# Kernel optimization log

Measured on AMD Instinct MI355X. Metric: run time of the kernel, lower is better.

## Reference

```python
import jax, jax.numpy as jnp
import numpy as np

N, P, T, D = 25000, 100000, 4, 128
DIN = 4 * D + 4  # 516
LEAKY = 0.001


def setup_inputs() -> dict:
    key = jax.random.key(0)
    ks = jax.random.split(key, 12)
    inp = {
        "coords": jax.random.normal(ks[0], (N, T, 3), jnp.float32),
        "propers": jax.random.randint(ks[1], (P, 4), 0, N, jnp.int64),
        "encoded": jax.random.normal(ks[2], (N, D), jnp.float32),
        "t": jax.random.uniform(ks[3], (T,), jnp.float32),
        "answer": jax.random.normal(ks[4], (N, T, 3), jnp.float32),
        # AggregateMLP(516 -> 128 -> 128 -> 128 -> 2), LeakyReLU(0.001) between
        "W0": jax.random.normal(ks[5], (DIN, D), jnp.float32) / np.sqrt(DIN),
        "b0": jnp.zeros((D,), jnp.float32),
        "W1": jax.random.normal(ks[6], (D, D), jnp.float32) / np.sqrt(D),
        "b1": jnp.zeros((D,), jnp.float32),
        "W2": jax.random.normal(ks[7], (D, D), jnp.float32) / np.sqrt(D),
        "b2": jnp.zeros((D,), jnp.float32),
        "W3": jax.random.normal(ks[8], (D, 2), jnp.float32) / np.sqrt(D),
        "b3": jnp.zeros((2,), jnp.float32),
    }
    return inp


def _forward(coords, propers, encoded, t, answer, W0, b0, W1, b1, W2, b2, W3, b3):
    p0, p1, p2, p3 = propers[:, 0], propers[:, 1], propers[:, 2], propers[:, 3]
    c0, c1, c2, c3 = coords[p0], coords[p1], coords[p2], coords[p3]  # [P,T,3]
    u1 = c1 - c0
    u2 = c2 - c1
    u3 = c3 - c2
    u1xu2 = jnp.cross(u1, u2, axis=-1)
    u2xu3 = jnp.cross(u2, u3, axis=-1)
    u2_norm = jnp.linalg.norm(u2, axis=-1, keepdims=True)
    u1yu2 = u1 * u2_norm
    theta = jnp.arctan2((u1yu2 * u2xu3).sum(-1), (u1xu2 * u2xu3).sum(-1))  # [P,T]
    dr = c0 - c3  # [P,T,3]
    dl = jnp.sqrt(jnp.clip(jnp.square(dr).sum(-1), 1e-12))  # [P,T]
    dh = dr / dl[..., None]

    Pn, Tn = propers.shape[0], t.shape[0]
    bcast = lambda e: jnp.broadcast_to(e[:, None, :], (Pn, Tn, e.shape[-1]))
    feats = jnp.concatenate(
        [
            bcast(encoded[p0]),
            bcast(encoded[p1]),
            bcast(encoded[p2]),
            bcast(encoded[p3]),
            jnp.broadcast_to(t.reshape(1, Tn, 1), (Pn, Tn, 1)),
            jnp.sin(theta)[..., None],
            jnp.cos(theta)[..., None],
            dl[..., None],
        ],
        axis=2,
    )  # [P,T,516]

    h = jax.nn.leaky_relu(feats @ W0 + b0, LEAKY)
    h = jax.nn.leaky_relu(h @ W1 + b1, LEAKY)
    h = jax.nn.leaky_relu(h @ W2 + b2, LEAKY)
    delta = h @ W3 + b3  # [P,T,2]

    out = answer.at[p0].add(-0.5 * delta[:, :, 0:1] * dh)
    out = out.at[p3].add(0.5 * delta[:, :, 1:2] * dh)
    return out


def reference(coords, propers, encoded, t, answer, W0, b0, W1, b1, W2, b2, W3, b3):
    return _forward(coords, propers, encoded, t, answer, W0, b0, W1, b1, W2, b2, W3, b3)
```

## Files before the change

kernel.cpp:

```cpp
#include <hip/hip_runtime.h>
#include <hip/hip_bf16.h>

#define NN 25000
#define PP 100000
#define TT 4
#define DD 128
#define LEAKY 0.001f

#define PB 32
#define ROWS 128

typedef __bf16 bf16;
typedef __bf16 bf16x8 __attribute__((ext_vector_type(8)));
typedef float  f32x4  __attribute__((ext_vector_type(4)));
typedef float  f32x2  __attribute__((ext_vector_type(2)));

#define OFF_W0SW  0u
#define OFF_W1SW  131072u
#define OFF_W2SW  163840u
#define OFF_W3SW  196608u
#define OFF_WTB   200704u
#define OFF_W5B   201728u
#define OFF_E     202496u
#define WS_END    25802496u

#define PR_W0SW  8192
#define PR_W1SW  2048
#define PR_W2SW  2048
#define PR_W3SW  256
#define PR_WTB   64
#define PR_W5B   48
#define PR_COPY4 75000
#define PR_TOTAL (PR_W0SW + PR_W1SW + PR_W2SW + PR_W3SW + PR_WTB + PR_W5B + PR_COPY4)

#define LGKM0() asm volatile("s_waitcnt lgkmcnt(0)" ::: "memory")

__device__ __forceinline__ void gload_lds16(const void* g, void* l) {
    __builtin_amdgcn_global_load_lds(
        (const __attribute__((address_space(1))) void*)g,
        (__attribute__((address_space(3))) void*)l, 16, 0, 0);
}

__global__ __launch_bounds__(256) void prep_kernel(
    const float* __restrict__ W0, const float* __restrict__ W1,
    const float* __restrict__ W2, const float* __restrict__ W3,
    const float* __restrict__ answer, const float* __restrict__ tvec,
    const float* __restrict__ b0,
    bf16* __restrict__ W0sw, bf16* __restrict__ W1sw, bf16* __restrict__ W2sw,
    bf16* __restrict__ W3sw, bf16* __restrict__ WtB, bf16* __restrict__ W5B,
    float* __restrict__ out)
{
    int idx = blockIdx.x * 256 + threadIdx.x;
    if (idx < PR_W0SW) {
        int lane = idx & 63, c = idx >> 6;
        int fr = lane & 15, quad = lane >> 4;
        int kc = c & 15, iwv = c >> 4;
        bf16 v[8];
        #pragma unroll
        for (int j = 0; j < 8; ++j)
            v[j] = (bf16)W0[(kc * 32 + quad * 8 + j) * 128 + iwv * 16 + fr];
        *(bf16x8*)(W0sw + c * 512 + lane * 8) = *(const bf16x8*)v;
        return;
    }
    idx -= PR_W0SW;
    if (idx < PR_W1SW) {
        int lane = idx & 63, c = idx >> 6;
        int fr = lane & 15, quad = lane >> 4;
        int kc = c & 3, nt = c >> 2;
        bf16 v[8];
        #pragma unroll
        for (int j = 0; j < 8; ++j)
            v[j] = (bf16)W1[(kc * 32 + quad * 8 + j) * 128 + nt * 16 + fr];
        *(bf16x8*)(W1sw + c * 512 + lane * 8) = *(const bf16x8*)v;
        return;
    }
    idx -= PR_W1SW;
    if (idx < PR_W2SW) {
        int lane = idx & 63, c = idx >> 6;
        int fr = lane & 15, quad = lane >> 4;
        int kc = c & 3, nt = c >> 2;
        bf16 v[8];
        #pragma unroll
        for (int j = 0; j < 8; ++j)
            v[j] = (bf16)W2[(kc * 32 + quad * 8 + j) * 128 + nt * 16 + fr];
        *(bf16x8*)(W2sw + c * 512 + lane * 8) = *(const bf16x8*)v;
        return;
    }
    idx -= PR_W2SW;
    if (idx < PR_W3SW) {
        int lane = idx & 63, kc = idx >> 6;
        int fr = lane & 15, quad = lane >> 4;
        bf16 v[8];
        #pragma unroll
        for (int j = 0; j < 8; ++j)
            v[j] = (fr < 2) ? (bf16)W3[(kc * 32 + quad * 8 + j) * 2 + fr] : (bf16)0.0f;
        *(bf16x8*)(W3sw + kc * 512 + lane * 8) = *(const bf16x8*)v;
        return;
    }
    idx -= PR_W3SW;
    if (idx < PR_WTB) {
        int t = idx >> 4, s = idx & 15;
        float tv = tvec[t];
        bf16 v[8];
        #pragma unroll
        for (int j = 0; j < 8; ++j)
            v[j] = (bf16)(tv * W0[512 * 128 + s * 8 + j] + b0[s * 8 + j]);
        *(bf16x8*)(WtB + t * 128 + s * 8) = *(const bf16x8*)v;
        return;
    }
    idx -= PR_WTB;
    if (idx < PR_W5B) {
        int r = idx >> 4, s = idx & 15;
        bf16 v[8];
        #pragma unroll
        for (int j = 0; j < 8; ++j)
            v[j] = (bf16)W0[(513 + r) * 128 + s * 8 + j];
        *(bf16x8*)(W5B + r * 128 + s * 8) = *(const bf16x8*)v;
        return;
    }
    idx -= PR_W5B;
    if (idx < PR_COPY4) { ((float4*)out)[idx] = ((const float4*)answer)[idx]; }
}

__global__ __launch_bounds__(256) void prep_e_kernel(
    const float* __restrict__ encoded, const bf16* __restrict__ W0sw,
    bf16* __restrict__ E)
{
    __shared__ bf16 sA[64][136];
    __shared__ bf16 sT[64][40];
    const int tid = threadIdx.x;
    const int row0 = (blockIdx.x >> 2) * 64;
    const int ntb  = blockIdx.x & 3;
    for (int c = tid; c < 2048; c += 256) {
        int row = c >> 5, seg = c & 31;
        int rr = row0 + row; if (rr >= NN) rr = NN - 1;
        float4 v = *(const float4*)(encoded + (size_t)rr * 128 + seg * 4);
        bf16 pk[4] = {(bf16)v.x, (bf16)v.y, (bf16)v.z, (bf16)v.w};
        *(uint2*)(&sA[row][seg * 4]) = *(const uint2*)pk;
    }
    __syncthreads();
    const int wv = tid >> 6, lane = tid & 63;
    const int fr = lane & 15, quad = lane >> 4;
    const bf16* aBase = &sA[wv * 16 + fr][quad * 8];
    bf16x8 aFv[4];
    #pragma unroll
    for (int kcc = 0; kcc < 4; ++kcc) aFv[kcc] = *(const bf16x8*)(aBase + kcc * 32);
    const int orow = tid >> 2, oseg = tid & 3;
    #pragma unroll
    for (int i = 0; i < 4; ++i) {
        #pragma unroll
        for (int ntl = 0; ntl < 2; ++ntl) {
            int nt = ntb * 2 + ntl;
            f32x4 acc = {0.f, 0.f, 0.f, 0.f};
            #pragma unroll
            for (int kcc = 0; kcc < 4; ++kcc) {
                bf16x8 bF = *(const bf16x8*)(W0sw + ((size_t)nt * 16 + i * 4 + kcc) * 512 + lane * 8);
                acc = __builtin_amdgcn_mfma_f32_16x16x32_bf16(aFv[kcc], bF, acc, 0, 0, 0);
            }
            #pragma unroll
            for (int reg = 0; reg < 4; ++reg)
                sT[wv * 16 + quad * 4 + reg][ntl * 16 + fr] = (bf16)acc[reg];
        }
        LGKM0();
        bf16x8 ev = *(const bf16x8*)(&sT[orow][oseg * 8]);
        LGKM0();
        if (row0 + orow < NN)
            *(bf16x8*)(E + ((size_t)i * NN + row0 + orow) * 128 + ntb * 32 + oseg * 8) = ev;
    }
}

__global__ __launch_bounds__(512, 4) void main_kernel(
    const float* __restrict__ coords, const int* __restrict__ propers,
    const float* __restrict__ b1, const float* __restrict__ b2,
    const float* __restrict__ b3,
    const bf16* __restrict__ E, const bf16* __restrict__ W1sw,
    const bf16* __restrict__ W2sw, const bf16* __restrict__ W3sw,
    const bf16* __restrict__ WtB, const bf16* __restrict__ W5B,
    float* __restrict__ out)
{
    __shared__ __align__(16) bf16 sH[8][16][136];
    __shared__ __align__(16) bf16 sW[18432];
    __shared__ float sScr[8][16][6];
    __shared__ int   sNd[8][8];

    const int tid  = threadIdx.x;
    const int wv   = tid >> 6, lane = tid & 63;
    const int fr   = lane & 15, quad = lane >> 4;
    const int pw   = blockIdx.x * PB + wv * 4;

    {
        const char* g1 = (const char*)W1sw;
        char* l = (char*)&sW[0];
        #pragma unroll
        for (int r2 = 0; r2 < 4; ++r2)
            gload_lds16(g1 + r2 * 8192 + wv * 1024 + lane * 16,
                        l + r2 * 8192 + wv * 1024);
        if (wv < 4)
            gload_lds16((const char*)W3sw + wv * 1024 + lane * 16,
                        l + 32768 + wv * 1024);
    }

    int4 pv = *(const int4*)(propers + (size_t)(pw + quad) * 4);
    bf16x8 e0 = *(const bf16x8*)(E + ((size_t)0 * NN + pv.x) * 128 + fr * 8);
    bf16x8 e1 = *(const bf16x8*)(E + ((size_t)1 * NN + pv.y) * 128 + fr * 8);
    bf16x8 e2 = *(const bf16x8*)(E + ((size_t)2 * NN + pv.z) * 128 + fr * 8);
    bf16x8 e3 = *(const bf16x8*)(E + ((size_t)3 * NN + pv.w) * 128 + fr * 8);
    if (fr == 0) { sNd[wv][quad * 2] = pv.x; sNd[wv][quad * 2 + 1] = pv.w; }
    bf16x8 w3v = *(const bf16x8*)(W5B + 0 * 128 + fr * 8);
    bf16x8 w4v = *(const bf16x8*)(W5B + 1 * 128 + fr * 8);
    bf16x8 w5v = *(const bf16x8*)(W5B + 2 * 128 + fr * 8);

    float b1r[8], b2r[8];
    #pragma unroll
    for (int i = 0; i < 8; ++i) {
        b1r[i] = b1[i * 16 + fr];
        b2r[i] = b2[i * 16 + fr];
    }
    float b3r = (fr < 2) ? b3[fr] : 0.0f;

    float snl = 0.f, csl = 1.f, dll = 0.f;
    if (lane < 16) {
        int pp_ = lane >> 2, t = lane & 3;
        int4 pg = *(const int4*)(propers + (size_t)(pw + pp_) * 4);
        const float* c0 = coords + (size_t)pg.x * 12 + t * 3;
        const float* c1 = coords + (size_t)pg.y * 12 + t * 3;
        const float* c2 = coords + (size_t)pg.z * 12 + t * 3;
        const float* c3 = coords + (size_t)pg.w * 12 + t * 3;
        float u1x = c1[0]-c0[0], u1y = c1[1]-c0[1], u1z = c1[2]-c0[2];
        float u2x = c2[0]-c1[0], u2y = c2[1]-c1[1], u2z = c2[2]-c1[2];
        float u3x = c3[0]-c2[0], u3y = c3[1]-c2[1], u3z = c3[2]-c2[2];
        float ax = u1y*u2z - u1z*u2y, ay = u1z*u2x - u1x*u2z, az = u1x*u2y - u1y*u2x;
        float bx = u2y*u3z - u2z*u3y, by = u2z*u3x - u2x*u3z, bz = u2x*u3y - u2y*u3x;
        float u2n = sqrtf(u2x*u2x + u2y*u2y + u2z*u2z);
        float num = u2n * (u1x*bx + u1y*by + u1z*bz);
        float den = ax*bx + ay*by + az*bz;
        float hyp = sqrtf(num*num + den*den);
        if (hyp > 1e-30f) { float ih = 1.0f / hyp; snl = num * ih; csl = den * ih; }
        else { snl = 0.0f; csl = 1.0f; }
        float drx = c0[0]-c3[0], dry = c0[1]-c3[1], drz = c0[2]-c3[2];
        dll = sqrtf(fmaxf(drx*drx + dry*dry + drz*drz, 1e-12f));
        float il = 1.0f / dll;
        sScr[wv][lane][0] = drx * il;
        sScr[wv][lane][1] = dry * il;
        sScr[wv][lane][2] = drz * il;
    }

    {
        f32x2 g2[4], w3f2[4], w4f2[4], w5f2[4];
        #pragma unroll
        for (int j = 0; j < 4; ++j) {
            g2[j] = (f32x2){
                (float)e0[2*j]   + (float)e1[2*j]   + (float)e2[2*j]   + (float)e3[2*j],
                (float)e0[2*j+1] + (float)e1[2*j+1] + (float)e2[2*j+1] + (float)e3[2*j+1] };
            w3f2[j] = (f32x2){ (float)w3v[2*j], (float)w3v[2*j+1] };
            w4f2[j] = (f32x2){ (float)w4v[2*j], (float)w4v[2*j+1] };
            w5f2[j] = (f32x2){ (float)w5v[2*j], (float)w5v[2*j+1] };
        }
        #pragma unroll
        for (int t = 0; t < 4; ++t) {
            int r = quad * 4 + t;
            bf16x8 wtv = *(const bf16x8*)(WtB + t * 128 + fr * 8);
            float sn = __shfl(snl, r), cs = __shfl(csl, r), dl = __shfl(dll, r);
            f32x2 sn2 = {sn, sn}, cs2 = {cs, cs}, dl2 = {dl, dl};
            bf16 hv[8];
            #pragma unroll
            for (int j = 0; j < 4; ++j) {
                f32x2 v = g2[j] + (f32x2){ (float)wtv[2*j], (float)wtv[2*j+1] };
                v = sn2 * w3f2[j] + v;
                v = cs2 * w4f2[j] + v;
                v = dl2 * w5f2[j] + v;
                f32x2 lv = v * LEAKY;
                v.x = fmaxf(v.x, lv.x);
                v.y = fmaxf(v.y, lv.y);
                hv[2*j]   = (bf16)v.x;
                hv[2*j+1] = (bf16)v.y;
            }
            *(bf16x8*)(&sH[wv][r][fr * 8]) = *(const bf16x8*)hv;
        }
    }
    __syncthreads();

#define DENSE_LAYER(BR)                                                         \
    {                                                                           \
        bf16x8 aF[4];                                                           \
        const bf16* aRow = &sH[wv][fr][quad * 8];                               \
        _Pragma("unroll")                                                       \
        for (int kc = 0; kc < 4; ++kc)                                          \
            aF[kc] = *(const bf16x8*)(aRow + kc * 32);                          \
        _Pragma("unroll")                                                       \
        for (int hh = 0; hh < 2; ++hh) {                                        \
            f32x4 acc[4];                                                       \
            _Pragma("unroll")                                                   \
            for (int nt = 0; nt < 4; ++nt) acc[nt] = (f32x4){0.f,0.f,0.f,0.f};  \
            __builtin_amdgcn_s_setprio(1);                                      \
            _Pragma("unroll")                                                   \
            for (int kc = 0; kc < 4; ++kc) {                                    \
                _Pragma("unroll")                                               \
                for (int nt = 0; nt < 4; ++nt) {                                \
                    bf16x8 bF = *(const bf16x8*)(sW +                           \
                        ((hh * 4 + nt) * 4 + kc) * 512 + lane * 8);             \
                    acc[nt] = __builtin_amdgcn_mfma_f32_16x16x32_bf16(          \
                        aF[kc], bF, acc[nt], 0, 0, 0);                          \
                }                                                               \
            }                                                                   \
            __builtin_amdgcn_s_setprio(0);                                      \
            _Pragma("unroll")                                                   \
            for (int nt = 0; nt < 4; ++nt) {                                    \
                int j = (hh * 4 + nt) * 16 + fr;                                \
                f32x4 v = acc[nt] + BR[hh * 4 + nt];                            \
                f32x4 lv = v * LEAKY;                                           \
                v.x = fmaxf(v.x, lv.x); v.y = fmaxf(v.y, lv.y);                 \
                v.z = fmaxf(v.z, lv.z); v.w = fmaxf(v.w, lv.w);                 \
                _Pragma("unroll")                                               \
                for (int reg = 0; reg < 4; ++reg)                               \
                    sH[wv][quad * 4 + reg][j] = (bf16)v[reg];                   \
            }                                                                   \
        }                                                                       \
    }

    DENSE_LAYER(b1r)
    __syncthreads();
    {
        const char* g2 = (const char*)W2sw;
        char* l = (char*)&sW[0];
        #pragma unroll
        for (int r2 = 0; r2 < 4; ++r2)
            gload_lds16(g2 + r2 * 8192 + wv * 1024 + lane * 16,
                        l + r2 * 8192 + wv * 1024);
    }
    __syncthreads();
    DENSE_LAYER(b2r)

    {
        bf16x8 aF[4];
        const bf16* aRow = &sH[wv][fr][quad * 8];
        #pragma unroll
        for (int kc = 0; kc < 4; ++kc)
            aF[kc] = *(const bf16x8*)(aRow + kc * 32);
        f32x4 dacc = {0.f, 0.f, 0.f, 0.f};
        __builtin_amdgcn_s_setprio(1);
        #pragma unroll
        for (int kc = 0; kc < 4; ++kc) {
            bf16x8 bF = *(const bf16x8*)(sW + 16384 + kc * 512 + lane * 8);
            dacc = __builtin_amdgcn_mfma_f32_16x16x32_bf16(aF[kc], bF, dacc, 0, 0, 0);
        }
        __builtin_amdgcn_s_setprio(0);
        if (fr < 2) {
            #pragma unroll
            for (int reg = 0; reg < 4; ++reg)
                sScr[wv][quad * 4 + reg][3 + fr] = dacc[reg] + b3r;
        }
    }

    {
        int row = lane & 15;
        int comp = lane >> 4;
        int side = (comp == 3) ? 1 : 0;
        int ax = side ? 0 : comp;
        int node = sNd[wv][(row >> 2) * 2 + side];
        float dval = (side ? 0.5f : -0.5f) * sScr[wv][row][3 + side];
        atomicAdd(out + (size_t)node * 12 + (row & 3) * 3 + ax, dval * sScr[wv][row][ax]);
        if (lane < 32) {
            int ax2 = 1 + comp;
            int node2 = sNd[wv][(row >> 2) * 2 + 1];
            float dval2 = 0.5f * sScr[wv][row][4];
            atomicAdd(out + (size_t)node2 * 12 + (row & 3) * 3 + ax2, dval2 * sScr[wv][row][ax2]);
        }
    }
#undef DENSE_LAYER
}

extern "C" void kernel_launch(void* const* d_in, const int* in_sizes, int n_in,
                              void* d_out, int out_size, void* d_ws, size_t ws_size,
                              hipStream_t stream) {
    const float* coords  = (const float*)d_in[0];
    const int*   propers = (const int*)d_in[1];
    const float* encoded = (const float*)d_in[2];
    const float* tvec    = (const float*)d_in[3];
    const float* answer  = (const float*)d_in[4];
    const float* W0 = (const float*)d_in[5];
    const float* b0 = (const float*)d_in[6];
    const float* W1 = (const float*)d_in[7];
    const float* b1 = (const float*)d_in[8];
    const float* W2 = (const float*)d_in[9];
    const float* b2 = (const float*)d_in[10];
    const float* W3 = (const float*)d_in[11];
    const float* b3 = (const float*)d_in[12];
    float* out = (float*)d_out;
    char* ws = (char*)d_ws;
    bf16* W0sw = (bf16*)(ws + OFF_W0SW);
    bf16* W1sw = (bf16*)(ws + OFF_W1SW);
    bf16* W2sw = (bf16*)(ws + OFF_W2SW);
    bf16* W3sw = (bf16*)(ws + OFF_W3SW);
    bf16* WtB  = (bf16*)(ws + OFF_WTB);
    bf16* W5B  = (bf16*)(ws + OFF_W5B);
    bf16* E    = (bf16*)(ws + OFF_E);

    int prep_blocks = (PR_TOTAL + 255) / 256;
    prep_kernel<<<prep_blocks, 256, 0, stream>>>(W0, W1, W2, W3, answer, tvec, b0,
                                                 W0sw, W1sw, W2sw, W3sw, WtB, W5B, out);
    prep_e_kernel<<<391 * 4, 256, 0, stream>>>(encoded, W0sw, E);
    main_kernel<<<PP / PB, 512, 0, stream>>>(coords, propers, b1, b2, b3,
                                             E, W1sw, W2sw, W3sw, WtB, W5B, out);
}
```

Measured before the change: 166.5 us.

## Make main kernel persistent with resident weights and prefetched next-chunk gathers

The main kernel now runs as a fixed grid of 256 blocks that loop over chunks of propers. All of W1, W2 and W3 are loaded into a larger LDS buffer once per block, which removes the per-block weight reloads and the mid-kernel barriers around the W2 swap. The propers indices, embedding rows and coordinates for the next chunk are issued before the current chunk's dense layers, so gather latency overlaps with MFMA work. In exchange there are fewer resident waves per CU, more register pressure, and a fixed grid size that may not balance evenly across CUs.

```diff
diff --git a/kernel.cpp b/kernel.cpp
--- a/kernel.cpp
+++ b/kernel.cpp
@@ -169,7 +169,7 @@
     }
 }
 
-__global__ __launch_bounds__(512, 4) void main_kernel(
+__global__ __launch_bounds__(512, 2) void main_kernel(
     const float* __restrict__ coords, const int* __restrict__ propers,
     const float* __restrict__ b1, const float* __restrict__ b2,
     const float* __restrict__ b3,
@@ -179,36 +179,17 @@
     float* __restrict__ out)
 {
     __shared__ __align__(16) bf16 sH[8][16][136];
-    __shared__ __align__(16) bf16 sW[18432];
+    __shared__ __align__(16) bf16 sW[34816];
     __shared__ float sScr[8][16][6];
     __shared__ int   sNd[8][8];
 
     const int tid  = threadIdx.x;
     const int wv   = tid >> 6, lane = tid & 63;
     const int fr   = lane & 15, quad = lane >> 4;
-    const int pw   = blockIdx.x * PB + wv * 4;
-
-    {
-        const char* g1 = (const char*)W1sw;
-        char* l = (char*)&sW[0];
-        #pragma unroll
-        for (int r2 = 0; r2 < 4; ++r2)
-            gload_lds16(g1 + r2 * 8192 + wv * 1024 + lane * 16,
-                        l + r2 * 8192 + wv * 1024);
-        if (wv < 4)
-            gload_lds16((const char*)W3sw + wv * 1024 + lane * 16,
-                        l + 32768 + wv * 1024);
-    }
-
-    int4 pv = *(const int4*)(propers + (size_t)(pw + quad) * 4);
-    bf16x8 e0 = *(const bf16x8*)(E + ((size_t)0 * NN + pv.x) * 128 + fr * 8);
-    bf16x8 e1 = *(const bf16x8*)(E + ((size_t)1 * NN + pv.y) * 128 + fr * 8);
-    bf16x8 e2 = *(const bf16x8*)(E + ((size_t)2 * NN + pv.z) * 128 + fr * 8);
-    bf16x8 e3 = *(const bf16x8*)(E + ((size_t)3 * NN + pv.w) * 128 + fr * 8);
-    if (fr == 0) { sNd[wv][quad * 2] = pv.x; sNd[wv][quad * 2 + 1] = pv.w; }
-    bf16x8 w3v = *(const bf16x8*)(W5B + 0 * 128 + fr * 8);
-    bf16x8 w4v = *(const bf16x8*)(W5B + 1 * 128 + fr * 8);
-    bf16x8 w5v = *(const bf16x8*)(W5B + 2 * 128 + fr * 8);
+
+    for (int i = wv; i < 68; i += 8)
+        gload_lds16((const char*)W1sw + (size_t)i * 1024 + lane * 16,
+                    (char*)sW + i * 1024);
 
     float b1r[8], b2r[8];
     #pragma unroll
@@ -217,70 +198,132 @@
         b2r[i] = b2[i * 16 + fr];
     }
     float b3r = (fr < 2) ? b3[fr] : 0.0f;
-
-    float snl = 0.f, csl = 1.f, dll = 0.f;
-    if (lane < 16) {
-        int pp_ = lane >> 2, t = lane & 3;
-        int4 pg = *(const int4*)(propers + (size_t)(pw + pp_) * 4);
-        const float* c0 = coords + (size_t)pg.x * 12 + t * 3;
-        const float* c1 = coords + (size_t)pg.y * 12 + t * 3;
-        const float* c2 = coords + (size_t)pg.z * 12 + t * 3;
-        const float* c3 = coords + (size_t)pg.w * 12 + t * 3;
-        float u1x = c1[0]-c0[0], u1y = c1[1]-c0[1], u1z = c1[2]-c0[2];
-        float u2x = c2[0]-c1[0], u2y = c2[1]-c1[1], u2z = c2[2]-c1[2];
-        float u3x = c3[0]-c2[0], u3y = c3[1]-c2[1], u3z = c3[2]-c2[2];
-        float ax = u1y*u2z - u1z*u2y, ay = u1z*u2x - u1x*u2z, az = u1x*u2y - u1y*u2x;
-        float bx = u2y*u3z - u2z*u3y, by = u2z*u3x - u2x*u3z, bz = u2x*u3y - u2y*u3x;
-        float u2n = sqrtf(u2x*u2x + u2y*u2y + u2z*u2z);
-        float num = u2n * (u1x*bx + u1y*by + u1z*bz);
-        float den = ax*bx + ay*by + az*bz;
-        float hyp = sqrtf(num*num + den*den);
-        if (hyp > 1e-30f) { float ih = 1.0f / hyp; snl = num * ih; csl = den * ih; }
-        else { snl = 0.0f; csl = 1.0f; }
-        float drx = c0[0]-c3[0], dry = c0[1]-c3[1], drz = c0[2]-c3[2];
-        dll = sqrtf(fmaxf(drx*drx + dry*dry + drz*drz, 1e-12f));
-        float il = 1.0f / dll;
-        sScr[wv][lane][0] = drx * il;
-        sScr[wv][lane][1] = dry * il;
-        sScr[wv][lane][2] = drz * il;
-    }
-
+    bf16x8 w3v = *(const bf16x8*)(W5B + 0 * 128 + fr * 8);
+    bf16x8 w4v = *(const bf16x8*)(W5B + 1 * 128 + fr * 8);
+    bf16x8 w5v = *(const bf16x8*)(W5B + 2 * 128 + fr * 8);
+    bf16x8 wtv[4];
+    #pragma unroll
+    for (int t = 0; t < 4; ++t) wtv[t] = *(const bf16x8*)(WtB + t * 128 + fr * 8);
+    f32x2 w3f2[4], w4f2[4], w5f2[4];
+    #pragma unroll
+    for (int j = 0; j < 4; ++j) {
+        w3f2[j] = (f32x2){ (float)w3v[2*j], (float)w3v[2*j+1] };
+        w4f2[j] = (f32x2){ (float)w4v[2*j], (float)w4v[2*j+1] };
+        w5f2[j] = (f32x2){ (float)w5v[2*j], (float)w5v[2*j+1] };
+    }
+
+    __syncthreads();
+
+    const int nChunks = PP / PB;
+    const int stride  = gridDim.x;
+    int chunk = blockIdx.x;
+
+    int4 pv; bf16x8 e0, e1, e2, e3; float cc[12];
     {
-        f32x2 g2[4], w3f2[4], w4f2[4], w5f2[4];
-        #pragma unroll
-        for (int j = 0; j < 4; ++j) {
-            g2[j] = (f32x2){
-                (float)e0[2*j]   + (float)e1[2*j]   + (float)e2[2*j]   + (float)e3[2*j],
-                (float)e0[2*j+1] + (float)e1[2*j+1] + (float)e2[2*j+1] + (float)e3[2*j+1] };
-            w3f2[j] = (f32x2){ (float)w3v[2*j], (float)w3v[2*j+1] };
-            w4f2[j] = (f32x2){ (float)w4v[2*j], (float)w4v[2*j+1] };
-            w5f2[j] = (f32x2){ (float)w5v[2*j], (float)w5v[2*j+1] };
-        }
-        #pragma unroll
-        for (int t = 0; t < 4; ++t) {
-            int r = quad * 4 + t;
-            bf16x8 wtv = *(const bf16x8*)(WtB + t * 128 + fr * 8);
-            float sn = __shfl(snl, r), cs = __shfl(csl, r), dl = __shfl(dll, r);
-            f32x2 sn2 = {sn, sn}, cs2 = {cs, cs}, dl2 = {dl, dl};
-            bf16 hv[8];
-            #pragma unroll
-            for (int j = 0; j < 4; ++j) {
-                f32x2 v = g2[j] + (f32x2){ (float)wtv[2*j], (float)wtv[2*j+1] };
-                v = sn2 * w3f2[j] + v;
-                v = cs2 * w4f2[j] + v;
-                v = dl2 * w5f2[j] + v;
-                f32x2 lv = v * LEAKY;
-                v.x = fmaxf(v.x, lv.x);
-                v.y = fmaxf(v.y, lv.y);
-                hv[2*j]   = (bf16)v.x;
-                hv[2*j+1] = (bf16)v.y;
-            }
-            *(bf16x8*)(&sH[wv][r][fr * 8]) = *(const bf16x8*)hv;
-        }
-    }
-    __syncthreads();
-
-#define DENSE_LAYER(BR)                                                         \
+        int pw = chunk * PB + wv * 4;
+        pv = *(const int4*)(propers + (size_t)(pw + quad) * 4);
+        e0 = *(const bf16x8*)(E + ((size_t)0 * NN + pv.x) * 128 + fr * 8);
+        e1 = *(const bf16x8*)(E + ((size_t)1 * NN + pv.y) * 128 + fr * 8);
+        e2 = *(const bf16x8*)(E + ((size_t)2 * NN + pv.z) * 128 + fr * 8);
+        e3 = *(const bf16x8*)(E + ((size_t)3 * NN + pv.w) * 128 + fr * 8);
+        if (lane < 16) {
+            int4 pg = *(const int4*)(propers + (size_t)(pw + (lane >> 2)) * 4);
+            int t = lane & 3;
+            const float* q0 = coords + (size_t)pg.x * 12 + t * 3;
+            const float* q1 = coords + (size_t)pg.y * 12 + t * 3;
+            const float* q2 = coords + (size_t)pg.z * 12 + t * 3;
+            const float* q3 = coords + (size_t)pg.w * 12 + t * 3;
+            cc[0]=q0[0]; cc[1]=q0[1]; cc[2]=q0[2];
+            cc[3]=q1[0]; cc[4]=q1[1]; cc[5]=q1[2];
+            cc[6]=q2[0]; cc[7]=q2[1]; cc[8]=q2[2];
+            cc[9]=q3[0]; cc[10]=q3[1]; cc[11]=q3[2];
+        }
+    }
+
+    while (true) {
+        const int next = chunk + stride;
+        const bool more = next < nChunks;
+
+        int4 pvn, pgn;
+        if (more) {
+            int pwn = next * PB + wv * 4;
+            pvn = *(const int4*)(propers + (size_t)(pwn + quad) * 4);
+            if (lane < 16)
+                pgn = *(const int4*)(propers + (size_t)(pwn + (lane >> 2)) * 4);
+        }
+
+        if (fr == 0) { sNd[wv][quad * 2] = pv.x; sNd[wv][quad * 2 + 1] = pv.w; }
+
+        float snl = 0.f, csl = 1.f, dll = 0.f;
+        if (lane < 16) {
+            float u1x = cc[3]-cc[0], u1y = cc[4]-cc[1], u1z = cc[5]-cc[2];
+            float u2x = cc[6]-cc[3], u2y = cc[7]-cc[4], u2z = cc[8]-cc[5];
+            float u3x = cc[9]-cc[6], u3y = cc[10]-cc[7], u3z = cc[11]-cc[8];
+            float ax = u1y*u2z - u1z*u2y, ay = u1z*u2x - u1x*u2z, az = u1x*u2y - u1y*u2x;
+            float bx = u2y*u3z - u2z*u3y, by = u2z*u3x - u2x*u3z, bz = u2x*u3y - u2y*u3x;
+            float u2n = sqrtf(u2x*u2x + u2y*u2y + u2z*u2z);
+            float num = u2n * (u1x*bx + u1y*by + u1z*bz);
+            float den = ax*bx + ay*by + az*bz;
+            float hyp = sqrtf(num*num + den*den);
+            if (hyp > 1e-30f) { float ih = 1.0f / hyp; snl = num * ih; csl = den * ih; }
+            else { snl = 0.0f; csl = 1.0f; }
+            float drx = cc[0]-cc[9], dry = cc[1]-cc[10], drz = cc[2]-cc[11];
+            dll = sqrtf(fmaxf(drx*drx + dry*dry + drz*drz, 1e-12f));
+            float il = 1.0f / dll;
+            sScr[wv][lane][0] = drx * il;
+            sScr[wv][lane][1] = dry * il;
+            sScr[wv][lane][2] = drz * il;
+        }
+
+        {
+            f32x2 g2[4];
+            #pragma unroll
+            for (int j = 0; j < 4; ++j)
+                g2[j] = (f32x2){
+                    (float)e0[2*j]   + (float)e1[2*j]   + (float)e2[2*j]   + (float)e3[2*j],
+                    (float)e0[2*j+1] + (float)e1[2*j+1] + (float)e2[2*j+1] + (float)e3[2*j+1] };
+            #pragma unroll
+            for (int t = 0; t < 4; ++t) {
+                int r = quad * 4 + t;
+                float sn = __shfl(snl, r), cs = __shfl(csl, r), dl = __shfl(dll, r);
+                f32x2 sn2 = {sn, sn}, cs2 = {cs, cs}, dl2 = {dl, dl};
+                bf16 hv[8];
+                #pragma unroll
+                for (int j = 0; j < 4; ++j) {
+                    f32x2 v = g2[j] + (f32x2){ (float)wtv[t][2*j], (float)wtv[t][2*j+1] };
+                    v = sn2 * w3f2[j] + v;
+                    v = cs2 * w4f2[j] + v;
+                    v = dl2 * w5f2[j] + v;
+                    f32x2 lv = v * LEAKY;
+                    v.x = fmaxf(v.x, lv.x);
+                    v.y = fmaxf(v.y, lv.y);
+                    hv[2*j]   = (bf16)v.x;
+                    hv[2*j+1] = (bf16)v.y;
+                }
+                *(bf16x8*)(&sH[wv][r][fr * 8]) = *(const bf16x8*)hv;
+            }
+        }
+
+        bf16x8 e0n, e1n, e2n, e3n; float ccn[12];
+        if (more) {
+            e0n = *(const bf16x8*)(E + ((size_t)0 * NN + pvn.x) * 128 + fr * 8);
+            e1n = *(const bf16x8*)(E + ((size_t)1 * NN + pvn.y) * 128 + fr * 8);
+            e2n = *(const bf16x8*)(E + ((size_t)2 * NN + pvn.z) * 128 + fr * 8);
+            e3n = *(const bf16x8*)(E + ((size_t)3 * NN + pvn.w) * 128 + fr * 8);
+            if (lane < 16) {
+                int t2 = lane & 3;
+                const float* q0 = coords + (size_t)pgn.x * 12 + t2 * 3;
+                const float* q1 = coords + (size_t)pgn.y * 12 + t2 * 3;
+                const float* q2 = coords + (size_t)pgn.z * 12 + t2 * 3;
+                const float* q3 = coords + (size_t)pgn.w * 12 + t2 * 3;
+                ccn[0]=q0[0]; ccn[1]=q0[1]; ccn[2]=q0[2];
+                ccn[3]=q1[0]; ccn[4]=q1[1]; ccn[5]=q1[2];
+                ccn[6]=q2[0]; ccn[7]=q2[1]; ccn[8]=q2[2];
+                ccn[9]=q3[0]; ccn[10]=q3[1]; ccn[11]=q3[2];
+            }
+        }
+
+#define DENSE_LAYER(OFFW, BR)                                                   \
     {                                                                           \
         bf16x8 aF[4];                                                           \
         const bf16* aRow = &sH[wv][fr][quad * 8];                               \
@@ -297,7 +340,7 @@
             for (int kc = 0; kc < 4; ++kc) {                                    \
                 _Pragma("unroll")                                               \
                 for (int nt = 0; nt < 4; ++nt) {                                \
-                    bf16x8 bF = *(const bf16x8*)(sW +                           \
+                    bf16x8 bF = *(const bf16x8*)(sW + OFFW +                    \
                         ((hh * 4 + nt) * 4 + kc) * 512 + lane * 8);             \
                     acc[nt] = __builtin_amdgcn_mfma_f32_16x16x32_bf16(          \
                         aF[kc], bF, acc[nt], 0, 0, 0);                          \
@@ -318,54 +361,53 @@
         }                                                                       \
     }
 
-    DENSE_LAYER(b1r)
-    __syncthreads();
-    {
-        const char* g2 = (const char*)W2sw;
-        char* l = (char*)&sW[0];
-        #pragma unroll
-        for (int r2 = 0; r2 < 4; ++r2)
-            gload_lds16(g2 + r2 * 8192 + wv * 1024 + lane * 16,
-                        l + r2 * 8192 + wv * 1024);
-    }
-    __syncthreads();
-    DENSE_LAYER(b2r)
-
-    {
-        bf16x8 aF[4];
-        const bf16* aRow = &sH[wv][fr][quad * 8];
-        #pragma unroll
-        for (int kc = 0; kc < 4; ++kc)
-            aF[kc] = *(const bf16x8*)(aRow + kc * 32);
-        f32x4 dacc = {0.f, 0.f, 0.f, 0.f};
-        __builtin_amdgcn_s_setprio(1);
-        #pragma unroll
-        for (int kc = 0; kc < 4; ++kc) {
-            bf16x8 bF = *(const bf16x8*)(sW + 16384 + kc * 512 + lane * 8);
-            dacc = __builtin_amdgcn_mfma_f32_16x16x32_bf16(aF[kc], bF, dacc, 0, 0, 0);
-        }
-        __builtin_amdgcn_s_setprio(0);
-        if (fr < 2) {
-            #pragma unroll
-            for (int reg = 0; reg < 4; ++reg)
-                sScr[wv][quad * 4 + reg][3 + fr] = dacc[reg] + b3r;
-        }
-    }
-
-    {
-        int row = lane & 15;
-        int comp = lane >> 4;
-        int side = (comp == 3) ? 1 : 0;
-        int ax = side ? 0 : comp;
-        int node = sNd[wv][(row >> 2) * 2 + side];
-        float dval = (side ? 0.5f : -0.5f) * sScr[wv][row][3 + side];
-        atomicAdd(out + (size_t)node * 12 + (row & 3) * 3 + ax, dval * sScr[wv][row][ax]);
-        if (lane < 32) {
-            int ax2 = 1 + comp;
-            int node2 = sNd[wv][(row >> 2) * 2 + 1];
-            float dval2 = 0.5f * sScr[wv][row][4];
-            atomicAdd(out + (size_t)node2 * 12 + (row & 3) * 3 + ax2, dval2 * sScr[wv][row][ax2]);
-        }
+        DENSE_LAYER(0, b1r)
+        DENSE_LAYER(16384, b2r)
+
+        {
+            bf16x8 aF[4];
+            const bf16* aRow = &sH[wv][fr][quad * 8];
+            #pragma unroll
+            for (int kc = 0; kc < 4; ++kc)
+                aF[kc] = *(const bf16x8*)(aRow + kc * 32);
+            f32x4 dacc = {0.f, 0.f, 0.f, 0.f};
+            __builtin_amdgcn_s_setprio(1);
+            #pragma unroll
+            for (int kc = 0; kc < 4; ++kc) {
+                bf16x8 bF = *(const bf16x8*)(sW + 32768 + kc * 512 + lane * 8);
+                dacc = __builtin_amdgcn_mfma_f32_16x16x32_bf16(aF[kc], bF, dacc, 0, 0, 0);
+            }
+            __builtin_amdgcn_s_setprio(0);
+            if (fr < 2) {
+                #pragma unroll
+                for (int reg = 0; reg < 4; ++reg)
+                    sScr[wv][quad * 4 + reg][3 + fr] = dacc[reg] + b3r;
+            }
+        }
+
+        {
+            int row = lane & 15;
+            int comp = lane >> 4;
+            int side = (comp == 3) ? 1 : 0;
+            int ax = side ? 0 : comp;
+            int node = sNd[wv][(row >> 2) * 2 + side];
+            float dval = (side ? 0.5f : -0.5f) * sScr[wv][row][3 + side];
+            atomicAdd(out + (size_t)node * 12 + (row & 3) * 3 + ax, dval * sScr[wv][row][ax]);
+            if (lane < 32) {
+                int ax2 = 1 + comp;
+                int node2 = sNd[wv][(row >> 2) * 2 + 1];
+                float dval2 = 0.5f * sScr[wv][row][4];
+                atomicAdd(out + (size_t)node2 * 12 + (row & 3) * 3 + ax2, dval2 * sScr[wv][row][ax2]);
+            }
+        }
+
+        if (!more) break;
+        pv = pvn; e0 = e0n; e1 = e1n; e2 = e2n; e3 = e3n;
+        if (lane < 16) {
+            #pragma unroll
+            for (int j = 0; j < 12; ++j) cc[j] = ccn[j];
+        }
+        chunk = next;
     }
 #undef DENSE_LAYER
 }
@@ -400,6 +442,6 @@
     prep_kernel<<<prep_blocks, 256, 0, stream>>>(W0, W1, W2, W3, answer, tvec, b0,
                                                  W0sw, W1sw, W2sw, W3sw, WtB, W5B, out);
     prep_e_kernel<<<391 * 4, 256, 0, stream>>>(encoded, W0sw, E);
-    main_kernel<<<PP / PB, 512, 0, stream>>>(coords, propers, b1, b2, b3,
-                                             E, W1sw, W2sw, W3sw, WtB, W5B, out);
+    main_kernel<<<256, 512, 0, stream>>>(coords, propers, b1, b2, b3,
+                                         E, W1sw, W2sw, W3sw, WtB, W5B, out);
 }
```

Result: slower. 174.9 us (+5.1%).

## Give each wave two 16-row M tiles to reuse weight fragments across rows

Applied to the files above, without the earlier changes.

Main kernel changes from 8 waves × 4 propers per wave to 4 waves × 8 propers per wave (256 threads, 32 rows each). Each LDS B-fragment load of the weights now feeds two MFMAs, one per M tile, so LDS traffic per MFMA is halved. The layer-0 gather and the scatter atomics are reorganised to match. The cost is more registers per wave and fewer waves per block, which may lower occupancy and latency hiding.

```diff
diff --git a/kernel.cpp b/kernel.cpp
--- a/kernel.cpp
+++ b/kernel.cpp
@@ -8,7 +8,9 @@
 #define LEAKY 0.001f
 
 #define PB 32
-#define ROWS 128
+#define WPB 4
+#define PPW 8
+#define RPW 32
 
 typedef __bf16 bf16;
 typedef __bf16 bf16x8 __attribute__((ext_vector_type(8)));
@@ -169,7 +171,7 @@
     }
 }
 
-__global__ __launch_bounds__(512, 4) void main_kernel(
+__global__ __launch_bounds__(256, 2) void main_kernel(
     const float* __restrict__ coords, const int* __restrict__ propers,
     const float* __restrict__ b1, const float* __restrict__ b2,
     const float* __restrict__ b3,
@@ -178,37 +180,46 @@
     const bf16* __restrict__ WtB, const bf16* __restrict__ W5B,
     float* __restrict__ out)
 {
-    __shared__ __align__(16) bf16 sH[8][16][136];
+    __shared__ __align__(16) bf16 sH[WPB][RPW][136];
     __shared__ __align__(16) bf16 sW[18432];
-    __shared__ float sScr[8][16][6];
-    __shared__ int   sNd[8][8];
+    __shared__ float sScr[WPB][RPW][6];
+    __shared__ int   sNd[WPB][16];
 
     const int tid  = threadIdx.x;
     const int wv   = tid >> 6, lane = tid & 63;
     const int fr   = lane & 15, quad = lane >> 4;
-    const int pw   = blockIdx.x * PB + wv * 4;
+    const int pw   = blockIdx.x * PB + wv * PPW;
 
     {
         const char* g1 = (const char*)W1sw;
-        char* l = (char*)&sW[0];
-        #pragma unroll
-        for (int r2 = 0; r2 < 4; ++r2)
-            gload_lds16(g1 + r2 * 8192 + wv * 1024 + lane * 16,
-                        l + r2 * 8192 + wv * 1024);
-        if (wv < 4)
-            gload_lds16((const char*)W3sw + wv * 1024 + lane * 16,
-                        l + 32768 + wv * 1024);
-    }
-
-    int4 pv = *(const int4*)(propers + (size_t)(pw + quad) * 4);
-    bf16x8 e0 = *(const bf16x8*)(E + ((size_t)0 * NN + pv.x) * 128 + fr * 8);
-    bf16x8 e1 = *(const bf16x8*)(E + ((size_t)1 * NN + pv.y) * 128 + fr * 8);
-    bf16x8 e2 = *(const bf16x8*)(E + ((size_t)2 * NN + pv.z) * 128 + fr * 8);
-    bf16x8 e3 = *(const bf16x8*)(E + ((size_t)3 * NN + pv.w) * 128 + fr * 8);
-    if (fr == 0) { sNd[wv][quad * 2] = pv.x; sNd[wv][quad * 2 + 1] = pv.w; }
+        #pragma unroll
+        for (int r8 = 0; r8 < 8; ++r8)
+            gload_lds16(g1 + (size_t)(r8 * WPB + wv) * 1024 + lane * 16,
+                        (char*)sW + (r8 * WPB + wv) * 1024);
+        gload_lds16((const char*)W3sw + (size_t)wv * 1024 + lane * 16,
+                    (char*)sW + 32768 + wv * 1024);
+    }
+
+    int4 pvA = *(const int4*)(propers + (size_t)(pw + quad) * 4);
+    int4 pvB = *(const int4*)(propers + (size_t)(pw + 4 + quad) * 4);
+    bf16x8 e0a = *(const bf16x8*)(E + ((size_t)0 * NN + pvA.x) * 128 + fr * 8);
+    bf16x8 e1a = *(const bf16x8*)(E + ((size_t)1 * NN + pvA.y) * 128 + fr * 8);
+    bf16x8 e2a = *(const bf16x8*)(E + ((size_t)2 * NN + pvA.z) * 128 + fr * 8);
+    bf16x8 e3a = *(const bf16x8*)(E + ((size_t)3 * NN + pvA.w) * 128 + fr * 8);
+    bf16x8 e0b = *(const bf16x8*)(E + ((size_t)0 * NN + pvB.x) * 128 + fr * 8);
+    bf16x8 e1b = *(const bf16x8*)(E + ((size_t)1 * NN + pvB.y) * 128 + fr * 8);
+    bf16x8 e2b = *(const bf16x8*)(E + ((size_t)2 * NN + pvB.z) * 128 + fr * 8);
+    bf16x8 e3b = *(const bf16x8*)(E + ((size_t)3 * NN + pvB.w) * 128 + fr * 8);
+    if (fr == 0) {
+        sNd[wv][quad * 2]     = pvA.x; sNd[wv][quad * 2 + 1]     = pvA.w;
+        sNd[wv][8 + quad * 2] = pvB.x; sNd[wv][8 + quad * 2 + 1] = pvB.w;
+    }
     bf16x8 w3v = *(const bf16x8*)(W5B + 0 * 128 + fr * 8);
     bf16x8 w4v = *(const bf16x8*)(W5B + 1 * 128 + fr * 8);
     bf16x8 w5v = *(const bf16x8*)(W5B + 2 * 128 + fr * 8);
+    bf16x8 wtv[4];
+    #pragma unroll
+    for (int t = 0; t < 4; ++t) wtv[t] = *(const bf16x8*)(WtB + t * 128 + fr * 8);
 
     float b1r[8], b2r[8];
     #pragma unroll
@@ -219,7 +230,7 @@
     float b3r = (fr < 2) ? b3[fr] : 0.0f;
 
     float snl = 0.f, csl = 1.f, dll = 0.f;
-    if (lane < 16) {
+    if (lane < 32) {
         int pp_ = lane >> 2, t = lane & 3;
         int4 pg = *(const int4*)(propers + (size_t)(pw + pp_) * 4);
         const float* c0 = coords + (size_t)pg.x * 12 + t * 3;
@@ -246,126 +257,142 @@
     }
 
     {
-        f32x2 g2[4], w3f2[4], w4f2[4], w5f2[4];
+        f32x2 w3f2[4], w4f2[4], w5f2[4];
         #pragma unroll
         for (int j = 0; j < 4; ++j) {
-            g2[j] = (f32x2){
-                (float)e0[2*j]   + (float)e1[2*j]   + (float)e2[2*j]   + (float)e3[2*j],
-                (float)e0[2*j+1] + (float)e1[2*j+1] + (float)e2[2*j+1] + (float)e3[2*j+1] };
             w3f2[j] = (f32x2){ (float)w3v[2*j], (float)w3v[2*j+1] };
             w4f2[j] = (f32x2){ (float)w4v[2*j], (float)w4v[2*j+1] };
             w5f2[j] = (f32x2){ (float)w5v[2*j], (float)w5v[2*j+1] };
         }
-        #pragma unroll
-        for (int t = 0; t < 4; ++t) {
-            int r = quad * 4 + t;
-            bf16x8 wtv = *(const bf16x8*)(WtB + t * 128 + fr * 8);
-            float sn = __shfl(snl, r), cs = __shfl(csl, r), dl = __shfl(dll, r);
-            f32x2 sn2 = {sn, sn}, cs2 = {cs, cs}, dl2 = {dl, dl};
-            bf16 hv[8];
-            #pragma unroll
-            for (int j = 0; j < 4; ++j) {
-                f32x2 v = g2[j] + (f32x2){ (float)wtv[2*j], (float)wtv[2*j+1] };
-                v = sn2 * w3f2[j] + v;
-                v = cs2 * w4f2[j] + v;
-                v = dl2 * w5f2[j] + v;
-                f32x2 lv = v * LEAKY;
-                v.x = fmaxf(v.x, lv.x);
-                v.y = fmaxf(v.y, lv.y);
-                hv[2*j]   = (bf16)v.x;
-                hv[2*j+1] = (bf16)v.y;
-            }
-            *(bf16x8*)(&sH[wv][r][fr * 8]) = *(const bf16x8*)hv;
+#define H0_PASS(E0, E1, E2, E3, RBASE)                                          \
+        {                                                                       \
+            f32x2 g2[4];                                                        \
+            _Pragma("unroll")                                                   \
+            for (int j = 0; j < 4; ++j)                                         \
+                g2[j] = (f32x2){                                                \
+                    (float)E0[2*j]   + (float)E1[2*j]   + (float)E2[2*j]   + (float)E3[2*j],   \
+                    (float)E0[2*j+1] + (float)E1[2*j+1] + (float)E2[2*j+1] + (float)E3[2*j+1] };\
+            _Pragma("unroll")                                                   \
+            for (int t = 0; t < 4; ++t) {                                       \
+                int r = (RBASE) + quad * 4 + t;                                 \
+                float sn = __shfl(snl, r), cs = __shfl(csl, r), dl = __shfl(dll, r); \
+                f32x2 sn2 = {sn, sn}, cs2 = {cs, cs}, dl2 = {dl, dl};           \
+                bf16 hv[8];                                                     \
+                _Pragma("unroll")                                               \
+                for (int j = 0; j < 4; ++j) {                                   \
+                    f32x2 v = g2[j] + (f32x2){ (float)wtv[t][2*j], (float)wtv[t][2*j+1] }; \
+                    v = sn2 * w3f2[j] + v;                                      \
+                    v = cs2 * w4f2[j] + v;                                      \
+                    v = dl2 * w5f2[j] + v;                                      \
+                    f32x2 lv = v * LEAKY;                                       \
+                    v.x = fmaxf(v.x, lv.x);                                     \
+                    v.y = fmaxf(v.y, lv.y);                                     \
+                    hv[2*j]   = (bf16)v.x;                                      \
+                    hv[2*j+1] = (bf16)v.y;                                      \
+                }                                                               \
+                *(bf16x8*)(&sH[wv][r][fr * 8]) = *(const bf16x8*)hv;            \
+            }                                                                   \
         }
+        H0_PASS(e0a, e1a, e2a, e3a, 0)
+        H0_PASS(e0b, e1b, e2b, e3b, 16)
+#undef H0_PASS
     }
     __syncthreads();
 
-#define DENSE_LAYER(BR)                                                         \
+#define DENSE_LAYER(OFFW, BR)                                                   \
     {                                                                           \
-        bf16x8 aF[4];                                                           \
-        const bf16* aRow = &sH[wv][fr][quad * 8];                               \
+        bf16x8 aF[2][4];                                                        \
         _Pragma("unroll")                                                       \
-        for (int kc = 0; kc < 4; ++kc)                                          \
-            aF[kc] = *(const bf16x8*)(aRow + kc * 32);                          \
+        for (int mt = 0; mt < 2; ++mt) {                                        \
+            const bf16* aRow = &sH[wv][mt * 16 + fr][quad * 8];                 \
+            _Pragma("unroll")                                                   \
+            for (int kc = 0; kc < 4; ++kc)                                      \
+                aF[mt][kc] = *(const bf16x8*)(aRow + kc * 32);                  \
+        }                                                                       \
         _Pragma("unroll")                                                       \
         for (int hh = 0; hh < 2; ++hh) {                                        \
-            f32x4 acc[4];                                                       \
-            _Pragma("unroll")                                                   \
-            for (int nt = 0; nt < 4; ++nt) acc[nt] = (f32x4){0.f,0.f,0.f,0.f};  \
+            f32x4 acc[2][4];                                                    \
+            _Pragma("unroll")                                                   \
+            for (int mt = 0; mt < 2; ++mt)                                      \
+                _Pragma("unroll")                                               \
+                for (int nt = 0; nt < 4; ++nt) acc[mt][nt] = (f32x4){0.f,0.f,0.f,0.f}; \
             __builtin_amdgcn_s_setprio(1);                                      \
             _Pragma("unroll")                                                   \
             for (int kc = 0; kc < 4; ++kc) {                                    \
                 _Pragma("unroll")                                               \
                 for (int nt = 0; nt < 4; ++nt) {                                \
-                    bf16x8 bF = *(const bf16x8*)(sW +                           \
+                    bf16x8 bF = *(const bf16x8*)(sW + OFFW +                    \
                         ((hh * 4 + nt) * 4 + kc) * 512 + lane * 8);             \
-                    acc[nt] = __builtin_amdgcn_mfma_f32_16x16x32_bf16(          \
-                        aF[kc], bF, acc[nt], 0, 0, 0);                          \
+                    acc[0][nt] = __builtin_amdgcn_mfma_f32_16x16x32_bf16(       \
+                        aF[0][kc], bF, acc[0][nt], 0, 0, 0);                    \
+                    acc[1][nt] = __builtin_amdgcn_mfma_f32_16x16x32_bf16(       \
+                        aF[1][kc], bF, acc[1][nt], 0, 0, 0);                    \
                 }                                                               \
             }                                                                   \
             __builtin_amdgcn_s_setprio(0);                                      \
             _Pragma("unroll")                                                   \
-            for (int nt = 0; nt < 4; ++nt) {                                    \
-                int j = (hh * 4 + nt) * 16 + fr;                                \
-                f32x4 v = acc[nt] + BR[hh * 4 + nt];                            \
-                f32x4 lv = v * LEAKY;                                           \
-                v.x = fmaxf(v.x, lv.x); v.y = fmaxf(v.y, lv.y);                 \
-                v.z = fmaxf(v.z, lv.z); v.w = fmaxf(v.w, lv.w);                 \
+            for (int mt = 0; mt < 2; ++mt)                                      \
                 _Pragma("unroll")                                               \
-                for (int reg = 0; reg < 4; ++reg)                               \
-                    sH[wv][quad * 4 + reg][j] = (bf16)v[reg];                   \
-            }                                                                   \
+                for (int nt = 0; nt < 4; ++nt) {                                \
+                    int j = (hh * 4 + nt) * 16 + fr;                            \
+                    f32x4 v = acc[mt][nt] + BR[hh * 4 + nt];                    \
+                    f32x4 lv = v * LEAKY;                                       \
+                    v.x = fmaxf(v.x, lv.x); v.y = fmaxf(v.y, lv.y);             \
+                    v.z = fmaxf(v.z, lv.z); v.w = fmaxf(v.w, lv.w);             \
+                    _Pragma("unroll")                                           \
+                    for (int reg = 0; reg < 4; ++reg)                           \
+                        sH[wv][mt * 16 + quad * 4 + reg][j] = (bf16)v[reg];     \
+                }                                                               \
         }                                                                       \
     }
 
-    DENSE_LAYER(b1r)
+    DENSE_LAYER(0, b1r)
     __syncthreads();
     {
         const char* g2 = (const char*)W2sw;
-        char* l = (char*)&sW[0];
-        #pragma unroll
-        for (int r2 = 0; r2 < 4; ++r2)
-            gload_lds16(g2 + r2 * 8192 + wv * 1024 + lane * 16,
-                        l + r2 * 8192 + wv * 1024);
+        #pragma unroll
+        for (int r8 = 0; r8 < 8; ++r8)
+            gload_lds16(g2 + (size_t)(r8 * WPB + wv) * 1024 + lane * 16,
+                        (char*)sW + (r8 * WPB + wv) * 1024);
     }
     __syncthreads();
-    DENSE_LAYER(b2r)
+    DENSE_LAYER(0, b2r)
 
     {
-        bf16x8 aF[4];
-        const bf16* aRow = &sH[wv][fr][quad * 8];
+        bf16x8 bW[4];
         #pragma unroll
         for (int kc = 0; kc < 4; ++kc)
-            aF[kc] = *(const bf16x8*)(aRow + kc * 32);
-        f32x4 dacc = {0.f, 0.f, 0.f, 0.f};
-        __builtin_amdgcn_s_setprio(1);
-        #pragma unroll
-        for (int kc = 0; kc < 4; ++kc) {
-            bf16x8 bF = *(const bf16x8*)(sW + 16384 + kc * 512 + lane * 8);
-            dacc = __builtin_amdgcn_mfma_f32_16x16x32_bf16(aF[kc], bF, dacc, 0, 0, 0);
+            bW[kc] = *(const bf16x8*)(sW + 16384 + kc * 512 + lane * 8);
+        #pragma unroll
+        for (int mt = 0; mt < 2; ++mt) {
+            bf16x8 aF[4];
+            const bf16* aRow = &sH[wv][mt * 16 + fr][quad * 8];
+            #pragma unroll
+            for (int kc = 0; kc < 4; ++kc)
+                aF[kc] = *(const bf16x8*)(aRow + kc * 32);
+            f32x4 dacc = {0.f, 0.f, 0.f, 0.f};
+            __builtin_amdgcn_s_setprio(1);
+            #pragma unroll
+            for (int kc = 0; kc < 4; ++kc)
+                dacc = __builtin_amdgcn_mfma_f32_16x16x32_bf16(aF[kc], bW[kc], dacc, 0, 0, 0);
+            __builtin_amdgcn_s_setprio(0);
+            if (fr < 2) {
+                #pragma unroll
+                for (int reg = 0; reg < 4; ++reg)
+                    sScr[wv][mt * 16 + quad * 4 + reg][3 + fr] = dacc[reg] + b3r;
+            }
         }
-        __builtin_amdgcn_s_setprio(0);
-        if (fr < 2) {
-            #pragma unroll
-            for (int reg = 0; reg < 4; ++reg)
-                sScr[wv][quad * 4 + reg][3 + fr] = dacc[reg] + b3r;
-        }
     }
 
     {
-        int row = lane & 15;
-        int comp = lane >> 4;
-        int side = (comp == 3) ? 1 : 0;
-        int ax = side ? 0 : comp;
+        int row  = lane & 31;
+        int side = lane >> 5;
         int node = sNd[wv][(row >> 2) * 2 + side];
         float dval = (side ? 0.5f : -0.5f) * sScr[wv][row][3 + side];
-        atomicAdd(out + (size_t)node * 12 + (row & 3) * 3 + ax, dval * sScr[wv][row][ax]);
-        if (lane < 32) {
-            int ax2 = 1 + comp;
-            int node2 = sNd[wv][(row >> 2) * 2 + 1];
-            float dval2 = 0.5f * sScr[wv][row][4];
-            atomicAdd(out + (size_t)node2 * 12 + (row & 3) * 3 + ax2, dval2 * sScr[wv][row][ax2]);
-        }
+        float* op = out + (size_t)node * 12 + (row & 3) * 3;
+        #pragma unroll
+        for (int ax = 0; ax < 3; ++ax)
+            atomicAdd(op + ax, dval * sScr[wv][row][ax]);
     }
 #undef DENSE_LAYER
 }
@@ -400,6 +427,6 @@
     prep_kernel<<<prep_blocks, 256, 0, stream>>>(W0, W1, W2, W3, answer, tvec, b0,
                                                  W0sw, W1sw, W2sw, W3sw, WtB, W5B, out);
     prep_e_kernel<<<391 * 4, 256, 0, stream>>>(encoded, W0sw, E);
-    main_kernel<<<PP / PB, 512, 0, stream>>>(coords, propers, b1, b2, b3,
+    main_kernel<<<PP / PB, 256, 0, stream>>>(coords, propers, b1, b2, b3,
                                              E, W1sw, W2sw, W3sw, WtB, W5B, out);
 }
```

After: 176.4 us. 6.0% more time.

## Use 10-wave blocks, keep W3 in registers, retile the E precompute

Applied to the files above, without the earlier changes.

The main kernel grows to 10 waves (40 propers) per block with launch bounds 640,5. The W3 fragment now lives in registers instead of LDS, which shrinks the shared weight buffer, and weight staging loops adapt to any wave count. The scatter epilogue becomes a generic 96-element loop. prep_e switches to 32-row tiles with each block covering half the output columns. Together these aim to raise occupancy and amortize weight loads, but they add register pressure and reduce per-wave parallelism in the prep kernel.

```diff
diff --git a/kernel.cpp b/kernel.cpp
--- a/kernel.cpp
+++ b/kernel.cpp
@@ -7,8 +7,8 @@
 #define DD 128
 #define LEAKY 0.001f
 
-#define PB 32
-#define ROWS 128
+#define PB 40
+#define WPB 10
 
 typedef __bf16 bf16;
 typedef __bf16 bf16x8 __attribute__((ext_vector_type(8)));
@@ -126,12 +126,12 @@
     const float* __restrict__ encoded, const bf16* __restrict__ W0sw,
     bf16* __restrict__ E)
 {
-    __shared__ bf16 sA[64][136];
-    __shared__ bf16 sT[64][40];
-    const int tid = threadIdx.x;
-    const int row0 = (blockIdx.x >> 2) * 64;
-    const int ntb  = blockIdx.x & 3;
-    for (int c = tid; c < 2048; c += 256) {
+    __shared__ bf16 sA[32][136];
+    __shared__ bf16 sT[32][72];
+    const int tid   = threadIdx.x;
+    const int row0  = (blockIdx.x >> 1) * 32;
+    const int nhalf = blockIdx.x & 1;
+    for (int c = tid; c < 1024; c += 256) {
         int row = c >> 5, seg = c & 31;
         int rr = row0 + row; if (rr >= NN) rr = NN - 1;
         float4 v = *(const float4*)(encoded + (size_t)rr * 128 + seg * 4);
@@ -141,16 +141,18 @@
     __syncthreads();
     const int wv = tid >> 6, lane = tid & 63;
     const int fr = lane & 15, quad = lane >> 4;
-    const bf16* aBase = &sA[wv * 16 + fr][quad * 8];
+    const int mt = wv >> 1, ch = wv & 1;
+    const bf16* aBase = &sA[mt * 16 + fr][quad * 8];
     bf16x8 aFv[4];
     #pragma unroll
     for (int kcc = 0; kcc < 4; ++kcc) aFv[kcc] = *(const bf16x8*)(aBase + kcc * 32);
-    const int orow = tid >> 2, oseg = tid & 3;
+    const int srow = mt * 16 + (lane >> 2);
+    const int scol = ch * 32 + (lane & 3) * 8;
     #pragma unroll
     for (int i = 0; i < 4; ++i) {
         #pragma unroll
         for (int ntl = 0; ntl < 2; ++ntl) {
-            int nt = ntb * 2 + ntl;
+            int nt = nhalf * 4 + ch * 2 + ntl;
             f32x4 acc = {0.f, 0.f, 0.f, 0.f};
             #pragma unroll
             for (int kcc = 0; kcc < 4; ++kcc) {
@@ -159,17 +161,18 @@
             }
             #pragma unroll
             for (int reg = 0; reg < 4; ++reg)
-                sT[wv * 16 + quad * 4 + reg][ntl * 16 + fr] = (bf16)acc[reg];
+                sT[mt * 16 + quad * 4 + reg][ch * 32 + ntl * 16 + fr] = (bf16)acc[reg];
         }
         LGKM0();
-        bf16x8 ev = *(const bf16x8*)(&sT[orow][oseg * 8]);
+        bf16x8 ev = *(const bf16x8*)(&sT[srow][scol]);
         LGKM0();
-        if (row0 + orow < NN)
-            *(bf16x8*)(E + ((size_t)i * NN + row0 + orow) * 128 + ntb * 32 + oseg * 8) = ev;
-    }
-}
-
-__global__ __launch_bounds__(512, 4) void main_kernel(
+        int rr = row0 + srow;
+        if (rr < NN)
+            *(bf16x8*)(E + ((size_t)i * NN + rr) * 128 + nhalf * 64 + scol) = ev;
+    }
+}
+
+__global__ __launch_bounds__(640, 5) void main_kernel(
     const float* __restrict__ coords, const int* __restrict__ propers,
     const float* __restrict__ b1, const float* __restrict__ b2,
     const float* __restrict__ b3,
@@ -178,27 +181,24 @@
     const bf16* __restrict__ WtB, const bf16* __restrict__ W5B,
     float* __restrict__ out)
 {
-    __shared__ __align__(16) bf16 sH[8][16][136];
-    __shared__ __align__(16) bf16 sW[18432];
-    __shared__ float sScr[8][16][6];
-    __shared__ int   sNd[8][8];
+    __shared__ __align__(16) bf16 sH[WPB][16][136];
+    __shared__ __align__(16) bf16 sW[16384];
+    __shared__ float sScr[WPB][16][6];
+    __shared__ int   sNd[WPB][8];
 
     const int tid  = threadIdx.x;
     const int wv   = tid >> 6, lane = tid & 63;
     const int fr   = lane & 15, quad = lane >> 4;
     const int pw   = blockIdx.x * PB + wv * 4;
 
-    {
-        const char* g1 = (const char*)W1sw;
-        char* l = (char*)&sW[0];
-        #pragma unroll
-        for (int r2 = 0; r2 < 4; ++r2)
-            gload_lds16(g1 + r2 * 8192 + wv * 1024 + lane * 16,
-                        l + r2 * 8192 + wv * 1024);
-        if (wv < 4)
-            gload_lds16((const char*)W3sw + wv * 1024 + lane * 16,
-                        l + 32768 + wv * 1024);
-    }
+    for (int i = wv; i < 32; i += WPB)
+        gload_lds16((const char*)W1sw + (size_t)i * 1024 + lane * 16,
+                    (char*)sW + i * 1024);
+
+    bf16x8 bW3[4];
+    #pragma unroll
+    for (int kc = 0; kc < 4; ++kc)
+        bW3[kc] = *(const bf16x8*)(W3sw + kc * 512 + lane * 8);
 
     int4 pv = *(const int4*)(propers + (size_t)(pw + quad) * 4);
     bf16x8 e0 = *(const bf16x8*)(E + ((size_t)0 * NN + pv.x) * 128 + fr * 8);
@@ -320,14 +320,9 @@
 
     DENSE_LAYER(b1r)
     __syncthreads();
-    {
-        const char* g2 = (const char*)W2sw;
-        char* l = (char*)&sW[0];
-        #pragma unroll
-        for (int r2 = 0; r2 < 4; ++r2)
-            gload_lds16(g2 + r2 * 8192 + wv * 1024 + lane * 16,
-                        l + r2 * 8192 + wv * 1024);
-    }
+    for (int i = wv; i < 32; i += WPB)
+        gload_lds16((const char*)W2sw + (size_t)i * 1024 + lane * 16,
+                    (char*)sW + i * 1024);
     __syncthreads();
     DENSE_LAYER(b2r)
 
@@ -340,10 +335,8 @@
         f32x4 dacc = {0.f, 0.f, 0.f, 0.f};
         __builtin_amdgcn_s_setprio(1);
         #pragma unroll
-        for (int kc = 0; kc < 4; ++kc) {
-            bf16x8 bF = *(const bf16x8*)(sW + 16384 + kc * 512 + lane * 8);
-            dacc = __builtin_amdgcn_mfma_f32_16x16x32_bf16(aF[kc], bF, dacc, 0, 0, 0);
-        }
+        for (int kc = 0; kc < 4; ++kc)
+            dacc = __builtin_amdgcn_mfma_f32_16x16x32_bf16(aF[kc], bW3[kc], dacc, 0, 0, 0);
         __builtin_amdgcn_s_setprio(0);
         if (fr < 2) {
             #pragma unroll
@@ -352,20 +345,12 @@
         }
     }
 
-    {
-        int row = lane & 15;
-        int comp = lane >> 4;
-        int side = (comp == 3) ? 1 : 0;
-        int ax = side ? 0 : comp;
-        int node = sNd[wv][(row >> 2) * 2 + side];
-        float dval = (side ? 0.5f : -0.5f) * sScr[wv][row][3 + side];
-        atomicAdd(out + (size_t)node * 12 + (row & 3) * 3 + ax, dval * sScr[wv][row][ax]);
-        if (lane < 32) {
-            int ax2 = 1 + comp;
-            int node2 = sNd[wv][(row >> 2) * 2 + 1];
-            float dval2 = 0.5f * sScr[wv][row][4];
-            atomicAdd(out + (size_t)node2 * 12 + (row & 3) * 3 + ax2, dval2 * sScr[wv][row][ax2]);
-        }
+    for (int idx = lane; idx < 96; idx += 64) {
+        int r = idx / 6, c = idx - (idx / 6) * 6;
+        int side = c / 3, ax = c - side * 3;
+        int node = sNd[wv][(r >> 2) * 2 + side];
+        float dval = (side ? 0.5f : -0.5f) * sScr[wv][r][3 + side];
+        atomicAdd(out + (size_t)node * 12 + (r & 3) * 3 + ax, dval * sScr[wv][r][ax]);
     }
 #undef DENSE_LAYER
 }
@@ -399,7 +384,7 @@
     int prep_blocks = (PR_TOTAL + 255) / 256;
     prep_kernel<<<prep_blocks, 256, 0, stream>>>(W0, W1, W2, W3, answer, tvec, b0,
                                                  W0sw, W1sw, W2sw, W3sw, WtB, W5B, out);
-    prep_e_kernel<<<391 * 4, 256, 0, stream>>>(encoded, W0sw, E);
-    main_kernel<<<PP / PB, 512, 0, stream>>>(coords, propers, b1, b2, b3,
+    prep_e_kernel<<<782 * 2, 256, 0, stream>>>(encoded, W0sw, E);
+    main_kernel<<<PP / PB, 640, 0, stream>>>(coords, propers, b1, b2, b3,
                                              E, W1sw, W2sw, W3sw, WtB, W5B, out);
 }
```

Result: slower. 220.5 us (+32.5%).
